# Kernel optimization log

Hardware: AMD Instinct MI355X
Metric: run time of the kernel (lower is better)

## Reference

```python
import jax, jax.numpy as jnp
import numpy as np


def matmul_hadU(x):
    """Fast Walsh-Hadamard transform along the last dim (power of 2),
    normalized by 1/sqrt(n) — faithful translation of QuaRot's matmul_hadU
    radix-2 butterfly loop (Sylvester-ordered Hadamard)."""
    shape = x.shape
    n = shape[-1]
    assert (n & (n - 1)) == 0, "last dim must be a power of 2"
    b = x.reshape(-1, n, 1)  # (rows, m, t) with m*t == n throughout
    m, t = n, 1
    while m > 1:
        b = b.reshape(-1, m // 2, 2, t)
        lo = b[:, :, 0, :]
        hi = b[:, :, 1, :]
        b = jnp.stack([lo + hi, lo - hi], axis=2).reshape(-1, m // 2, 2 * t)
        m //= 2
        t *= 2
    scale = jnp.asarray(1.0 / np.sqrt(n), dtype=x.dtype)
    return b.reshape(shape) * scale


def setup_inputs() -> dict:
    key = jax.random.key(0)
    k1, k2, k3 = jax.random.split(key, 3)
    d = 2048
    x = jax.random.normal(k1, (4, 4096, d), dtype=jnp.float32)
    W = jax.random.normal(k2, (d, d), dtype=jnp.float32) * (1.0 / np.sqrt(d))
    b = jax.random.normal(k3, (d,), dtype=jnp.float32) * 0.01
    return {"x": x, "W": W, "b": b}


def reference(x, W, b):
    # R4Wrapper.forward: Hadamard-rotate x, then wrapped nn.Linear
    xr = matmul_hadU(x)                 # [B, S, D]
    return jnp.einsum("bsd,od->bso", xr, W) + b
```

## Files before the change

### kernel.cpp

```cpp
#include <hip/hip_runtime.h>
#include <stdint.h>

typedef __bf16 bf16x8 __attribute__((ext_vector_type(8)));
typedef float  f32x4  __attribute__((ext_vector_type(8/2)));

__device__ __forceinline__ unsigned short f2bf(float f) {
    union { float f; unsigned int u; } v; v.f = f;
    unsigned int u = v.u;
    return (unsigned short)((u + 0x7FFFu + ((u >> 16) & 1u)) >> 16);
}

__global__ void cast_x_kernel(const float4* __restrict__ X,
                              ushort4* __restrict__ A, int n4) {
    int i = blockIdx.x * blockDim.x + threadIdx.x;
    if (i < n4) {
        float4 v = X[i];
        ushort4 o;
        o.x = f2bf(v.x); o.y = f2bf(v.y); o.z = f2bf(v.z); o.w = f2bf(v.w);
        A[i] = o;
    }
}

__global__ void fwht_w_kernel(const float* __restrict__ W,
                              unsigned short* __restrict__ Bt) {
    const int n = 2048;
    __shared__ float buf[2048];
    const float* src = W + (size_t)blockIdx.x * n;
    for (int i = threadIdx.x; i < n; i += 256) buf[i] = src[i];
    __syncthreads();
    for (int len = 1; len < n; len <<= 1) {
        for (int j = threadIdx.x; j < n / 2; j += 256) {
            int idx = ((j & ~(len - 1)) << 1) | (j & (len - 1));
            float a = buf[idx], b = buf[idx + len];
            buf[idx]       = a + b;
            buf[idx + len] = a - b;
        }
        __syncthreads();
    }
    const float scale = 0.02209708691207961f;
    unsigned short* dst = Bt + (size_t)blockIdx.x * n;
    for (int i = threadIdx.x; i < n; i += 256) dst[i] = f2bf(buf[i] * scale);
}

__global__ __launch_bounds__(256) void had_gemm_kernel(
    const unsigned short* __restrict__ A,
    const unsigned short* __restrict__ B,
    const float* __restrict__ bias,
    float* __restrict__ C,
    int M, int N, int K)
{
    __shared__ __attribute__((aligned(16))) unsigned short As[128 * 32];
    __shared__ __attribute__((aligned(16))) unsigned short Bs[128 * 32];

    const int tid  = threadIdx.x;
    const int lane = tid & 63;
    const int wave = tid >> 6;
    const int m0 = blockIdx.y * 128;
    const int n0 = blockIdx.x * 128;
    const int wm = (wave & 1) * 64;
    const int wn = (wave >> 1) * 64;
    const int l16  = lane & 15;
    const int quad = lane >> 4;

    f32x4 acc[4][4] = {};

    const int u0 = (wave * 2 + 0) * 64 + lane;
    const int u1 = (wave * 2 + 1) * 64 + lane;
    const unsigned short* gA0 = A + (size_t)(m0 + (u0 >> 2)) * K + (u0 & 3) * 8;
    const unsigned short* gA1 = A + (size_t)(m0 + (u1 >> 2)) * K + (u1 & 3) * 8;
    const unsigned short* gB0 = B + (size_t)(n0 + (u0 >> 2)) * K + (u0 & 3) * 8;
    const unsigned short* gB1 = B + (size_t)(n0 + (u1 >> 2)) * K + (u1 & 3) * 8;
    unsigned short* lA0 = As + (wave * 2 + 0) * 512;
    unsigned short* lA1 = As + (wave * 2 + 1) * 512;
    unsigned short* lB0 = Bs + (wave * 2 + 0) * 512;
    unsigned short* lB1 = Bs + (wave * 2 + 1) * 512;

    const unsigned short* pa = As + (wm + l16) * 32 + quad * 8;
    const unsigned short* pb = Bs + (wn + l16) * 32 + quad * 8;

    for (int k0 = 0; k0 < K; k0 += 32) {
        __builtin_amdgcn_global_load_lds(
            (__attribute__((address_space(1))) void*)(gA0 + k0),
            (__attribute__((address_space(3))) void*)lA0, 16, 0, 0);
        __builtin_amdgcn_global_load_lds(
            (__attribute__((address_space(1))) void*)(gA1 + k0),
            (__attribute__((address_space(3))) void*)lA1, 16, 0, 0);
        __builtin_amdgcn_global_load_lds(
            (__attribute__((address_space(1))) void*)(gB0 + k0),
            (__attribute__((address_space(3))) void*)lB0, 16, 0, 0);
        __builtin_amdgcn_global_load_lds(
            (__attribute__((address_space(1))) void*)(gB1 + k0),
            (__attribute__((address_space(3))) void*)lB1, 16, 0, 0);
        __syncthreads();

        bf16x8 af[4], bfr[4];
        #pragma unroll
        for (int i = 0; i < 4; ++i) af[i]  = *(const bf16x8*)(pa + i * 512);
        #pragma unroll
        for (int j = 0; j < 4; ++j) bfr[j] = *(const bf16x8*)(pb + j * 512);
        #pragma unroll
        for (int i = 0; i < 4; ++i)
            #pragma unroll
            for (int j = 0; j < 4; ++j)
                acc[i][j] = __builtin_amdgcn_mfma_f32_16x16x32_bf16(
                    af[i], bfr[j], acc[i][j], 0, 0, 0);
        __syncthreads();
    }

    float bv[4];
    #pragma unroll
    for (int j = 0; j < 4; ++j) bv[j] = bias[n0 + wn + j * 16 + l16];

    #pragma unroll
    for (int i = 0; i < 4; ++i) {
        #pragma unroll
        for (int r = 0; r < 4; ++r) {
            int row = m0 + wm + i * 16 + quad * 4 + r;
            float* cp = C + (size_t)row * N + (n0 + wn + l16);
            #pragma unroll
            for (int j = 0; j < 4; ++j)
                cp[j * 16] = acc[i][j][r] + bv[j];
        }
    }
}

extern "C" void kernel_launch(void* const* d_in, const int* in_sizes, int n_in,
                              void* d_out, int out_size, void* d_ws, size_t ws_size,
                              hipStream_t stream) {
    const float* x = (const float*)d_in[0];
    const float* W = (const float*)d_in[1];
    const float* b = (const float*)d_in[2];
    float* out = (float*)d_out;

    const int d = in_sizes[2];
    const int M = in_sizes[0] / d;
    const int N = d, K = d;

    unsigned short* A_ws  = (unsigned short*)d_ws;
    unsigned short* Bt_ws = A_ws + (size_t)M * K;

    int n4 = in_sizes[0] / 4;
    cast_x_kernel<<<(n4 + 255) / 256, 256, 0, stream>>>(
        (const float4*)x, (ushort4*)A_ws, n4);

    fwht_w_kernel<<<N, 256, 0, stream>>>(W, Bt_ws);

    dim3 grid(N / 128, M / 128);
    had_gemm_kernel<<<grid, 256, 0, stream>>>(A_ws, Bt_ws, b, out, M, N, K);
}
```

Measured before the change: 408.2 us.

## Fuse fp32-to-bf16 cast of x into GEMM tile loads

Drops the separate cast kernel and has the GEMM load fp32 x tiles straight into LDS, converting to bf16 in registers before the MFMA. This removes one full write and read of a bf16 copy of x plus a kernel launch. In exchange the GEMM fetches twice as many bytes of A per tile, every N-block re-reads fp32 A, and LDS use and per-iteration conversion work go up.

```diff
diff --git a/kernel.cpp b/kernel.cpp
--- a/kernel.cpp
+++ b/kernel.cpp
@@ -2,23 +2,13 @@
 #include <stdint.h>
 
 typedef __bf16 bf16x8 __attribute__((ext_vector_type(8)));
-typedef float  f32x4  __attribute__((ext_vector_type(8/2)));
+typedef float  f32x4  __attribute__((ext_vector_type(4)));
+typedef float  f32x8  __attribute__((ext_vector_type(8)));
 
 __device__ __forceinline__ unsigned short f2bf(float f) {
     union { float f; unsigned int u; } v; v.f = f;
     unsigned int u = v.u;
     return (unsigned short)((u + 0x7FFFu + ((u >> 16) & 1u)) >> 16);
-}
-
-__global__ void cast_x_kernel(const float4* __restrict__ X,
-                              ushort4* __restrict__ A, int n4) {
-    int i = blockIdx.x * blockDim.x + threadIdx.x;
-    if (i < n4) {
-        float4 v = X[i];
-        ushort4 o;
-        o.x = f2bf(v.x); o.y = f2bf(v.y); o.z = f2bf(v.z); o.w = f2bf(v.w);
-        A[i] = o;
-    }
 }
 
 __global__ void fwht_w_kernel(const float* __restrict__ W,
@@ -43,13 +33,13 @@
 }
 
 __global__ __launch_bounds__(256) void had_gemm_kernel(
-    const unsigned short* __restrict__ A,
+    const float* __restrict__ A,
     const unsigned short* __restrict__ B,
     const float* __restrict__ bias,
     float* __restrict__ C,
     int M, int N, int K)
 {
-    __shared__ __attribute__((aligned(16))) unsigned short As[128 * 32];
+    __shared__ __attribute__((aligned(16))) float          Asf[128 * 32];
     __shared__ __attribute__((aligned(16))) unsigned short Bs[128 * 32];
 
     const int tid  = threadIdx.x;
@@ -64,38 +54,50 @@
 
     f32x4 acc[4][4] = {};
 
-    const int u0 = (wave * 2 + 0) * 64 + lane;
-    const int u1 = (wave * 2 + 1) * 64 + lane;
-    const unsigned short* gA0 = A + (size_t)(m0 + (u0 >> 2)) * K + (u0 & 3) * 8;
-    const unsigned short* gA1 = A + (size_t)(m0 + (u1 >> 2)) * K + (u1 & 3) * 8;
-    const unsigned short* gB0 = B + (size_t)(n0 + (u0 >> 2)) * K + (u0 & 3) * 8;
-    const unsigned short* gB1 = B + (size_t)(n0 + (u1 >> 2)) * K + (u1 & 3) * 8;
-    unsigned short* lA0 = As + (wave * 2 + 0) * 512;
-    unsigned short* lA1 = As + (wave * 2 + 1) * 512;
-    unsigned short* lB0 = Bs + (wave * 2 + 0) * 512;
-    unsigned short* lB1 = Bs + (wave * 2 + 1) * 512;
+    const float* gA[4];
+    float* lA[4];
+    #pragma unroll
+    for (int c = 0; c < 4; ++c) {
+        int u = wave * 4 + c;
+        int row = u * 8 + (lane >> 3);
+        gA[c] = A + (size_t)(m0 + row) * K + (lane & 7) * 4;
+        lA[c] = Asf + u * 256;
+    }
+    const unsigned short* gB[2];
+    unsigned short* lB[2];
+    #pragma unroll
+    for (int c = 0; c < 2; ++c) {
+        int u = wave * 2 + c;
+        int row = u * 16 + (lane >> 2);
+        gB[c] = B + (size_t)(n0 + row) * K + (lane & 3) * 8;
+        lB[c] = Bs + u * 512;
+    }
 
-    const unsigned short* pa = As + (wm + l16) * 32 + quad * 8;
-    const unsigned short* pb = Bs + (wn + l16) * 32 + quad * 8;
+    const float*          pa = Asf + (wm + l16) * 32 + quad * 8;
+    const unsigned short* pb = Bs  + (wn + l16) * 32 + quad * 8;
 
     for (int k0 = 0; k0 < K; k0 += 32) {
-        __builtin_amdgcn_global_load_lds(
-            (__attribute__((address_space(1))) void*)(gA0 + k0),
-            (__attribute__((address_space(3))) void*)lA0, 16, 0, 0);
-        __builtin_amdgcn_global_load_lds(
-            (__attribute__((address_space(1))) void*)(gA1 + k0),
-            (__attribute__((address_space(3))) void*)lA1, 16, 0, 0);
-        __builtin_amdgcn_global_load_lds(
-            (__attribute__((address_space(1))) void*)(gB0 + k0),
-            (__attribute__((address_space(3))) void*)lB0, 16, 0, 0);
-        __builtin_amdgcn_global_load_lds(
-            (__attribute__((address_space(1))) void*)(gB1 + k0),
-            (__attribute__((address_space(3))) void*)lB1, 16, 0, 0);
+        #pragma unroll
+        for (int c = 0; c < 4; ++c)
+            __builtin_amdgcn_global_load_lds(
+                (__attribute__((address_space(1))) const void*)(gA[c] + k0),
+                (__attribute__((address_space(3))) void*)lA[c], 16, 0, 0);
+        #pragma unroll
+        for (int c = 0; c < 2; ++c)
+            __builtin_amdgcn_global_load_lds(
+                (__attribute__((address_space(1))) const void*)(gB[c] + k0),
+                (__attribute__((address_space(3))) void*)lB[c], 16, 0, 0);
         __syncthreads();
 
         bf16x8 af[4], bfr[4];
         #pragma unroll
-        for (int i = 0; i < 4; ++i) af[i]  = *(const bf16x8*)(pa + i * 512);
+        for (int i = 0; i < 4; ++i) {
+            f32x8 a32 = *(const f32x8*)(pa + i * 512);
+            bf16x8 r;
+            #pragma unroll
+            for (int e = 0; e < 8; ++e) r[e] = (__bf16)a32[e];
+            af[i] = r;
+        }
         #pragma unroll
         for (int j = 0; j < 4; ++j) bfr[j] = *(const bf16x8*)(pb + j * 512);
         #pragma unroll
@@ -136,15 +138,10 @@
     const int M = in_sizes[0] / d;
     const int N = d, K = d;
 
-    unsigned short* A_ws  = (unsigned short*)d_ws;
-    unsigned short* Bt_ws = A_ws + (size_t)M * K;
-
-    int n4 = in_sizes[0] / 4;
-    cast_x_kernel<<<(n4 + 255) / 256, 256, 0, stream>>>(
-        (const float4*)x, (ushort4*)A_ws, n4);
+    unsigned short* Bt_ws = (unsigned short*)d_ws;
 
     fwht_w_kernel<<<N, 256, 0, stream>>>(W, Bt_ws);
 
     dim3 grid(N / 128, M / 128);
-    had_gemm_kernel<<<grid, 256, 0, stream>>>(A_ws, Bt_ws, b, out, M, N, K);
+    had_gemm_kernel<<<grid, 256, 0, stream>>>(x, Bt_ws, b, out, M, N, K);
 }
```

After: 464.8 us. +13.9%, slower.
